# Optimization experiments

Measured on AMD Instinct MI355X. Metric: run time of the kernel, lower is better.

## Reference

```python
import jax, jax.numpy as jnp
import numpy as np

N_ORDER = 256      # HiPPO order (window_size=[256])
OUT_LEN = 96       # output_window_size
IN_LEN = 720       # input_window_size
MULTISCALE = [1, 2, 4]
MODES = 32         # min(32, min(OUT_LEN, IN_LEN)//2)
EPS = 1e-5


def _transition(N):
    Q = np.arange(N, dtype=np.float64)
    R = (2 * Q + 1)[:, None]
    j, i = np.meshgrid(Q, Q)
    A = np.where(i < j, -1.0, (-1.0) ** (i - j + 1)) * R
    B = (-1.0) ** Q[:, None] * R
    return A, B


def _bilinear_discretize(A, B, dt):
    # scipy cont2discrete(method='bilinear'): Ad = (I - dt/2 A)^-1 (I + dt/2 A), Bd = (I - dt/2 A)^-1 dt B
    n = A.shape[0]
    I = np.eye(n)
    ima = I - 0.5 * dt * A
    Ad = np.linalg.solve(ima, I + 0.5 * dt * A)
    Bd = np.linalg.solve(ima, dt * B)
    return Ad, Bd.squeeze(-1)


def _eval_legendre(N, x):
    # Legendre P_n(x), n=0..N-1, via three-term recurrence. Returns [len(x), N].
    P = np.zeros((N, x.shape[0]))
    P[0] = 1.0
    if N > 1:
        P[1] = x
    for n in range(1, N - 1):
        P[n + 1] = ((2 * n + 1) * x * P[n] - n * P[n - 1]) / (n + 1)
    return P.T


def setup_inputs() -> dict:
    key = jax.random.key(0)
    ks = jax.random.split(key, 4)
    B, L, E = 16, IN_LEN, 64
    x = jax.random.normal(ks[0], (B, L, E), dtype=jnp.float32)
    scale = 1.0 / (N_ORDER * N_ORDER)
    wr = scale * jax.random.uniform(ks[1], (3, N_ORDER, N_ORDER, MODES), dtype=jnp.float32)
    wi = scale * jax.random.uniform(ks[2], (3, N_ORDER, N_ORDER, MODES), dtype=jnp.float32)
    mlp_w = 0.1 * jax.random.normal(ks[3], (1, 3), dtype=jnp.float32)
    mlp_b = jnp.zeros((1,), dtype=jnp.float32)
    A_c, B_c = _transition(N_ORDER)
    Ads, Bds, evs = [], [], []
    for m in MULTISCALE:
        dt = 1.0 / OUT_LEN / m
        Ad, Bd = _bilinear_discretize(A_c, B_c, dt)
        vals = np.arange(0.0, 1.0, dt)
        ev = _eval_legendre(N_ORDER, 1.0 - 2.0 * vals)  # [m*OUT_LEN, N]
        Ads.append(Ad); Bds.append(Bd); evs.append(ev[-OUT_LEN:])
    A = jnp.asarray(np.stack(Ads), dtype=jnp.float32)          # [3,N,N]
    Bv = jnp.asarray(np.stack(Bds), dtype=jnp.float32)         # [3,N]
    eval_last = jnp.asarray(np.stack(evs), dtype=jnp.float32)  # [3,OUT_LEN,N]
    return {"x": x, "wr": wr, "wi": wi, "mlp_w": mlp_w, "mlp_b": mlp_b,
            "A": A, "Bv": Bv, "eval_last": eval_last}


def _hippo(xin, Ad, Bd):
    # xin: [B,E,T] -> states [B,E,N,T]; c_t = A c_{t-1} + B f_t
    c0 = jnp.zeros(xin.shape[:2] + (Ad.shape[0],), xin.dtype)
    def step(c, f):  # f: [B,E]
        c = c @ Ad.T + f[..., None] * Bd
        return c, c
    _, cs = jax.lax.scan(step, c0, jnp.moveaxis(xin, -1, 0))  # [T,B,E,N]
    return jnp.transpose(cs, (1, 2, 3, 0))


def _spec_conv(xc, wr, wi):
    # xc: [B,E,N,T]; FFT -> low-mode complex channel mix -> iFFT
    T = xc.shape[-1]
    x_ft = jnp.fft.rfft(xc)                 # [B,E,N,T//2+1]
    a = x_ft[..., :MODES]
    w = (wr + 1j * wi).astype(a.dtype)      # [N,N,MODES]
    out = jnp.einsum('bjix,iox->bjox', a, w)
    nf = T // 2 + 1
    out_ft = jnp.pad(out, ((0, 0), (0, 0), (0, 0), (0, nf - MODES)))
    return jnp.fft.irfft(out_ft, n=T)       # [B,E,N,T]


def reference(x, wr, wi, mlp_w, mlp_b, A, Bv, eval_last):
    # instance standard scale (RevIN-style, no affine)
    mean = jnp.mean(x, axis=1, keepdims=True)            # [B,1,E]
    std = jnp.sqrt(jnp.var(x, axis=1, keepdims=True) + EPS)
    xn = (x - mean) / std
    xe = jnp.transpose(xn, (0, 2, 1))                    # [B,E,L]
    decs = []
    for s, m in enumerate(MULTISCALE):
        T = m * OUT_LEN
        x_in = xe[:, :, -T:]
        xc = _hippo(x_in, A[s], Bv[s])                   # [B,E,N,T]
        out1 = _spec_conv(xc, wr[s], wi[s])              # [B,E,N,T]
        x_dec_c = out1[:, :, :, OUT_LEN - 1]             # [B,E,N]  (input >= output branch, jump_dist=0)
        decs.append(x_dec_c @ eval_last[s].T)            # [B,E,OUT_LEN]
    xd = jnp.stack(decs, axis=-1)                        # [B,E,OUT,3]
    xd = (xd @ mlp_w.T + mlp_b)[..., 0]                  # [B,E,OUT]
    xd = jnp.transpose(xd, (0, 2, 1))                    # [B,OUT,E]
    return xd * std + mean
```

## Files before the change

kernel.cpp:

```cpp
#include <hip/hip_runtime.h>

typedef unsigned short u16;
typedef unsigned int u32;

typedef __bf16 bf16x8 __attribute__((ext_vector_type(8)));
typedef unsigned short ushort8 __attribute__((ext_vector_type(8)));
typedef float f32x16 __attribute__((ext_vector_type(16)));

#define STATSP 2048
#define EPOFF 32768
#define KKOFF0 591872
#define KKOFF1 616448
#define KKOFF2 665600
#define WOFF 763904
#define R0OFF 5482496
#define R1OFF 6072320
#define R2OFF 7251968
#define HTOTOFF 11675648
#define AD64 0
#define PD64 196608
#define KKD64 589824

__device__ __forceinline__ u32 pack_hl(float a) {
  u32 bits = __builtin_bit_cast(u32, a);
  u32 hi = (bits + 0x7fffu + ((bits >> 16) & 1u)) >> 16;
  float hif = __builtin_bit_cast(float, hi << 16);
  float r = a - hif;
  u32 lo = __builtin_bit_cast(u32, r) >> 16;
  return hi | (lo << 16);
}

__device__ __forceinline__ void unpk8(const u32* p, bf16x8& h, bf16x8& l) {
  ushort8 hu, lu;
#pragma unroll
  for (int j = 0; j < 8; ++j) {
    u32 v = p[j];
    hu[j] = (unsigned short)(v & 0xffffu);
    lu[j] = (unsigned short)(v >> 16);
  }
  h = __builtin_bit_cast(bf16x8, hu);
  l = __builtin_bit_cast(bf16x8, lu);
}

__global__ __launch_bounds__(256) void k_pre(const float* __restrict__ Ab,
                                             const float* __restrict__ Bb,
                                             const float* __restrict__ xin,
                                             const float* __restrict__ ev,
                                             float* __restrict__ ws) {
  __shared__ float rs[4][64], rq[4][64];
  int blk = blockIdx.x, tid = threadIdx.x;
  if (blk < 771) {
    double* dws = (double*)(ws + WOFF);
    int idx = blk * 256 + tid;
    if (idx < 196608) {
      dws[AD64 + idx] = (double)Ab[idx];
    } else {
      int g = idx - 196608;
      const int rowoff[3] = {0, 24576, 73728};
      const int kko[3] = {KKOFF0, KKOFF1, KKOFF2};
      int s = g >> 8, i = g & 255;
      float v = Bb[g];
      dws[KKD64 + rowoff[s] + i] = (double)v;
      ((u32*)ws)[kko[s] + i] = pack_hl(v);
    }
  } else if (blk < 963) {
    int b2 = blk - 771;
    int b = b2 / 12, part = b2 % 12;
    int j = tid & 63, g = tid >> 6;
    const float* xp = xin + ((size_t)b * 720 + part * 60 + g) * 64 + j;
    float sum = 0.f, ss = 0.f;
#pragma unroll
    for (int i = 0; i < 15; ++i) {
      float v = xp[(size_t)i * 256];
      sum += v; ss += v * v;
    }
    rs[g][j] = sum; rq[g][j] = ss;
    __syncthreads();
    if (g == 0) {
      float s = rs[0][j] + rs[1][j] + rs[2][j] + rs[3][j];
      float q = rq[0][j] + rq[1][j] + rq[2][j] + rq[3][j];
      float* dst = ws + STATSP + ((size_t)b2 * 64 + j) * 2;
      dst[0] = s; dst[1] = q;
    }
  } else if (blk < 987) {
    int idx = (blk - 963) * 256 + tid;
    for (; idx < 36864; idx += 24 * 256) ws[HTOTOFF + idx] = 0.f;
  } else {
    int idx = (blk - 987) * 256 + tid;
    ((u32*)ws)[EPOFF + idx] = pack_hl(ev[idx]);
  }
}

struct G64Jobs {
  const double* A[8]; const double* B[8]; double* C[8]; float* CF[8];
  int M[8]; int transB[8]; int tile0[8];
  int njobs;
};

__global__ __launch_bounds__(256) void k_gemm64(G64Jobs jb) {
  int bid = blockIdx.x;
  int j = 0;
  for (int q = 1; q < jb.njobs; ++q) if (bid >= jb.tile0[q]) j = q;
  int local = bid - jb.tile0[j];
  int tm = local >> 3, tn = local & 7;
  const double* A = jb.A[j];
  const double* Bm = jb.B[j];
  double* C = jb.C[j];
  float* CF = jb.CF[j];
  int M = jb.M[j], tB = jb.transB[j];
  int row0 = tm * 32, col0 = tn * 32;
  __shared__ double As[32][33], Bs[32][33];
  int tid = threadIdx.x;
  int ty = tid >> 4, tx = tid & 15;
  int lr = tid >> 3, lk = (tid & 7) << 2;
  double va[4], vb[4];
#pragma unroll
  for (int u = 0; u < 4; ++u) {
    va[u] = (row0 + lr < M) ? A[(size_t)(row0 + lr) * 256 + lk + u] : 0.0;
    vb[u] = tB ? Bm[(size_t)(col0 + lr) * 256 + lk + u]
               : Bm[(size_t)lr * 256 + col0 + lk + u];
  }
  double a00 = 0., a01 = 0., a10 = 0., a11 = 0.;
  for (int kc = 0; kc < 256; kc += 32) {
#pragma unroll
    for (int u = 0; u < 4; ++u) {
      As[lr][lk + u] = va[u];
      if (tB) Bs[lk + u][lr] = vb[u];
      else    Bs[lr][lk + u] = vb[u];
    }
    __syncthreads();
    if (kc < 224) {
      int kn = kc + 32;
#pragma unroll
      for (int u = 0; u < 4; ++u) {
        va[u] = (row0 + lr < M) ? A[(size_t)(row0 + lr) * 256 + kn + lk + u] : 0.0;
        vb[u] = tB ? Bm[(size_t)(col0 + lr) * 256 + kn + lk + u]
                   : Bm[(size_t)(kn + lr) * 256 + col0 + lk + u];
      }
    }
#pragma unroll 8
    for (int k = 0; k < 32; ++k) {
      double x0 = As[2 * ty][k], x1 = As[2 * ty + 1][k];
      double y0 = Bs[k][2 * tx], y1 = Bs[k][2 * tx + 1];
      a00 = fma(x0, y0, a00); a01 = fma(x0, y1, a01);
      a10 = fma(x1, y0, a10); a11 = fma(x1, y1, a11);
    }
    __syncthreads();
  }
  int r0 = row0 + 2 * ty, c0 = col0 + 2 * tx;
  if (r0 < M) {
    C[(size_t)r0 * 256 + c0] = a00; C[(size_t)r0 * 256 + c0 + 1] = a01;
    if (CF) {
      ((u32*)CF)[(size_t)r0 * 256 + c0] = pack_hl((float)a00);
      ((u32*)CF)[(size_t)r0 * 256 + c0 + 1] = pack_hl((float)a01);
    }
  }
  if (r0 + 1 < M) {
    C[(size_t)(r0 + 1) * 256 + c0] = a10; C[(size_t)(r0 + 1) * 256 + c0 + 1] = a11;
    if (CF) {
      ((u32*)CF)[(size_t)(r0 + 1) * 256 + c0] = pack_hl((float)a10);
      ((u32*)CF)[(size_t)(r0 + 1) * 256 + c0 + 1] = pack_hl((float)a11);
    }
  }
}

__global__ __launch_bounds__(256, 3) void k_s3(const float* __restrict__ wr,
                                               const float* __restrict__ wi,
                                               float* __restrict__ ws) {
  __shared__ float ms[64 * 97];
  int bid = blockIdx.x;
  int jidx = bid >> 7;
  int r127 = bid & 127;
  int mb = ((r127 & 7) << 4) | (r127 >> 3);
  int s = jidx >> 1, p = jidx & 1;
  const float* w = (p ? wi : wr) + (size_t)s * 2097152;
  const u32* ep = (const u32*)ws + EPOFF + s * 24576;
  int i0 = mb * 2;
  int tid = threadIdx.x;
  int lane = tid & 63;
  int wid = tid >> 6;
  int il = wid & 1, kh = wid >> 1;

  int tcol = lane & 31;
  int og8 = (lane >> 5) << 3;
  const float* aw0 = w + (((size_t)(i0 + il) * 256 + kh * 128 + og8) << 5) + tcol;
  const u32* bsrc = ep + tcol * 256 + og8;

  f32x16 acc[3];
#pragma unroll
  for (int f = 0; f < 3; ++f)
#pragma unroll
    for (int r = 0; r < 16; ++r) acc[f][r] = 0.f;

#pragma unroll 2
  for (int c = 0; c < 4; ++c) {
    int ko = kh * 128 + c * 32;
#pragma unroll
    for (int ks = 0; ks < 2; ++ks) {
      const float* aw = aw0 + ((c * 32 + ks * 16) << 5);
      u32 ap[8];
#pragma unroll
      for (int j2 = 0; j2 < 8; ++j2) ap[j2] = pack_hl(aw[(size_t)j2 << 5]);
      bf16x8 ah, al;
      unpk8(ap, ah, al);
#pragma unroll
      for (int f = 0; f < 3; ++f) {
        const uint4* bq = (const uint4*)(bsrc + f * 8192 + ko + ks * 16);
        uint4 b0 = bq[0], b1 = bq[1];
        u32 bp[8] = {b0.x, b0.y, b0.z, b0.w, b1.x, b1.y, b1.z, b1.w};
        bf16x8 bh, bl;
        unpk8(bp, bh, bl);
        acc[f] = __builtin_amdgcn_mfma_f32_32x32x16_bf16(ah, bh, acc[f], 0, 0, 0);
        acc[f] = __builtin_amdgcn_mfma_f32_32x32x16_bf16(ah, bl, acc[f], 0, 0, 0);
        acc[f] = __builtin_amdgcn_mfma_f32_32x32x16_bf16(al, bh, acc[f], 0, 0, 0);
      }
    }
  }

  int crow0 = (lane >> 5) << 2;
  if (kh == 1) {
#pragma unroll
    for (int f = 0; f < 3; ++f)
#pragma unroll
      for (int r = 0; r < 16; ++r) {
        int row = il * 32 + crow0 + (r & 3) + ((r >> 2) << 3);
        ms[row * 97 + f * 32 + tcol] = acc[f][r];
      }
  }
  __syncthreads();
  if (kh == 0) {
#pragma unroll
    for (int f = 0; f < 3; ++f)
#pragma unroll
      for (int r = 0; r < 16; ++r) {
        int row = il * 32 + crow0 + (r & 3) + ((r >> 2) << 3);
        int a = row * 97 + f * 32 + tcol;
        ms[a] += acc[f][r];
      }
  }
  __syncthreads();
  u32* W2 = (u32*)(ws + WOFF) + (size_t)jidx * 786432 + (size_t)(mb >> 2) * 24576 +
            ((mb & 3) << 1);
  int x = tid & 31, cg = tid >> 5;
#pragma unroll
  for (int j = 0; j < 12; ++j) {
    int c = cg * 12 + j;
    float v0 = ms[x * 97 + c];
    float v1 = ms[(32 + x) * 97 + c];
    uint2 st;
    st.x = pack_hl(v0);
    st.y = pack_hl(v1);
    *(uint2*)(W2 + (size_t)(x * 96 + c) * 8) = st;
  }
}

__global__ __launch_bounds__(256) void k_s4(float* __restrict__ ws) {
  int bid = blockIdx.x;
  const int cums[6] = {0, 36, 72, 144, 216, 360};
  int jidx = 0;
#pragma unroll
  for (int q = 1; q < 6; ++q) if (bid >= cums[q]) jidx = q;
  int local = bid - cums[jidx];
  int s = jidx >> 1, p = jidx & 1;
  const int Ts[3] = {96, 192, 384};
  const int KKo[3] = {KKOFF0, KKOFF1, KKOFF2};
  const int Ro[3] = {R0OFF, R1OFF, R2OFF};
  int T = Ts[s];
  int td = local / 12, tn = local % 12;
  int d0 = td * 32;
  int tid = threadIdx.x;
  int lane = tid & 63, wid = tid >> 6;
  int n0 = tn * 256 + wid * 64;
  int l31 = lane & 31, kg = lane >> 5;
  const u32* Ap = (const u32*)ws + KKo[s] + (size_t)(d0 + l31) * 256 + kg * 8;
  const u32* Bp = (const u32*)ws + WOFF + (size_t)jidx * 786432 + (size_t)kg * 24576;
  const u32* b0p = Bp + (size_t)(n0 + l31) * 8;
  const u32* b1p = Bp + (size_t)(n0 + 32 + l31) * 8;
  float* C = ws + Ro[s] + (size_t)p * T * 3072;

  f32x16 acc0, acc1;
#pragma unroll
  for (int r = 0; r < 16; ++r) { acc0[r] = 0.f; acc1[r] = 0.f; }

#pragma unroll 2
  for (int ks = 0; ks < 16; ++ks) {
    uint4 a0 = *(const uint4*)(Ap + ks * 16);
    uint4 a1 = *(const uint4*)(Ap + ks * 16 + 4);
    size_t bo = (size_t)ks * 49152;
    uint4 x0 = *(const uint4*)(b0p + bo);
    uint4 x1 = *(const uint4*)(b0p + bo + 4);
    uint4 y0 = *(const uint4*)(b1p + bo);
    uint4 y1 = *(const uint4*)(b1p + bo + 4);
    u32 ap[8] = {a0.x, a0.y, a0.z, a0.w, a1.x, a1.y, a1.z, a1.w};
    bf16x8 ah, al;
    unpk8(ap, ah, al);
    {
      u32 bp[8] = {x0.x, x0.y, x0.z, x0.w, x1.x, x1.y, x1.z, x1.w};
      bf16x8 bh, bl;
      unpk8(bp, bh, bl);
      acc0 = __builtin_amdgcn_mfma_f32_32x32x16_bf16(ah, bh, acc0, 0, 0, 0);
      acc0 = __builtin_amdgcn_mfma_f32_32x32x16_bf16(ah, bl, acc0, 0, 0, 0);
      acc0 = __builtin_amdgcn_mfma_f32_32x32x16_bf16(al, bh, acc0, 0, 0, 0);
      acc0 = __builtin_amdgcn_mfma_f32_32x32x16_bf16(al, bl, acc0, 0, 0, 0);
    }
    {
      u32 bp[8] = {y0.x, y0.y, y0.z, y0.w, y1.x, y1.y, y1.z, y1.w};
      bf16x8 bh, bl;
      unpk8(bp, bh, bl);
      acc1 = __builtin_amdgcn_mfma_f32_32x32x16_bf16(ah, bh, acc1, 0, 0, 0);
      acc1 = __builtin_amdgcn_mfma_f32_32x32x16_bf16(ah, bl, acc1, 0, 0, 0);
      acc1 = __builtin_amdgcn_mfma_f32_32x32x16_bf16(al, bh, acc1, 0, 0, 0);
      acc1 = __builtin_amdgcn_mfma_f32_32x32x16_bf16(al, bl, acc1, 0, 0, 0);
    }
  }

  int crow = kg << 2;
#pragma unroll
  for (int r = 0; r < 16; ++r) {
    int row = d0 + crow + (r & 3) + ((r >> 2) << 3);
    C[(size_t)row * 3072 + n0 + l31] = acc0[r];
    C[(size_t)row * 3072 + n0 + 32 + l31] = acc1[r];
  }
}

__global__ __launch_bounds__(192) void k_s5a(const float* __restrict__ mlpw, float* __restrict__ ws) {
  int bid = blockIdx.x;
  int s = bid >> 7;
  int rem = bid & 127;
  int x = rem >> 2;
  int tq = rem & 3;
  const int Ts[3] = {96, 192, 384};
  const int Ro[3] = {R0OFF, R1OFF, R2OFF};
  const int lpbase[3] = {288, 192, 0};
  int T = Ts[s];
  int Lc = T >> 3;
  __shared__ float cs[384][2];
  __shared__ float Lsr[8][24], Lsi[8][24];
  int tid = threadIdx.x;
  for (int e = tid; e < T; e += 192) {
    float th = 6.283185307179586f * (float)e / (float)T;
    cs[e][0] = cosf(th);
    cs[e][1] = sinf(th);
  }
  int c = tid / 24, tl = tid % 24;
  int t = tq * 24 + tl;
  const float* Rre = ws + Ro[s] + (size_t)x * 96 + t;
  const float* Rim = Rre + (size_t)T * 3072;
  float* Htot = ws + HTOTOFF;
  float wsc = mlpw[s];
  __syncthreads();
  int d0 = c * Lc;
  float zr = 0.f, zi = 0.f;
  for (int d = d0; d < d0 + Lc; ++d) {
    float rr = Rre[(size_t)d * 3072];
    float ri = Rim[(size_t)d * 3072];
    int e1 = (x * d) % T;
    float c1 = cs[e1][0], s1 = cs[e1][1];
    zr += c1 * rr + s1 * ri;
    zi += c1 * ri - s1 * rr;
  }
  Lsr[c][tl] = zr; Lsi[c][tl] = zi;
  __syncthreads();
  if (c == 0) {
    float pr = 0.f, pi = 0.f;
#pragma unroll
    for (int cc = 0; cc < 8; ++cc) {
      float lr = Lsr[cc][tl], li = Lsi[cc][tl];
      Lsr[cc][tl] = pr; Lsi[cc][tl] = pi;
      pr += lr; pi += li;
    }
  }
  __syncthreads();
  zr = Lsr[c][tl]; zi = Lsi[c][tl];
  float sc = (((x == 0) ? 1.f : 2.f) / (float)T) * wsc;
  for (int d = d0; d < d0 + Lc; ++d) {
    float rr = Rre[(size_t)d * 3072];
    float ri = Rim[(size_t)d * 3072];
    int e1 = (x * d) % T;
    float c1 = cs[e1][0], s1 = cs[e1][1];
    zr += c1 * rr + s1 * ri;
    zi += c1 * ri - s1 * rr;
    int k = T - 1 - d;
    int e2 = (x * (95 - k)) % T;
    if (e2 < 0) e2 += T;
    float c2 = cs[e2][0], s2 = cs[e2][1];
    atomicAdd(Htot + (size_t)(lpbase[s] + k) * 96 + t, sc * (c2 * zr - s2 * zi));
  }
}

__global__ __launch_bounds__(256) void k_s6(const float* __restrict__ xin, const float* __restrict__ mlpb_p,
                                            const float* __restrict__ ws, float* __restrict__ out) {
  int b = blockIdx.x >> 2, tq = blockIdx.x & 3;
  int tid = threadIdx.x;
  int j = tid & 63, tsub = tid >> 6;
  __shared__ float Ht[384 * 24];
  for (int idx = tid; idx < 384 * 24; idx += 256) {
    int lp = idx / 24, c = idx % 24;
    Ht[idx] = ws[HTOTOFF + lp * 96 + tq * 24 + c];
  }
  float ssum = 0.f, sq = 0.f;
#pragma unroll
  for (int p = 0; p < 12; ++p) {
    const float* src = ws + STATSP + (((size_t)b * 12 + p) * 64 + j) * 2;
    ssum += src[0]; sq += src[1];
  }
  float mn = ssum * (1.f / 720.f);
  float var = sq * (1.f / 720.f) - mn * mn;
  float sd = sqrtf(var + 1e-5f);
  __syncthreads();
  float mlpb = mlpb_p[0];
  float acc[6] = {0.f, 0.f, 0.f, 0.f, 0.f, 0.f};
  float accS[6] = {0.f, 0.f, 0.f, 0.f, 0.f, 0.f};
  const float* xp = xin + ((size_t)b * 720 + 336) * 64 + j;
  for (int lp = 0; lp < 384; ++lp) {
    float xv = xp[(size_t)lp * 64];
    const float* hr = &Ht[lp * 24 + tsub * 6];
    float2 h01 = *(const float2*)&hr[0];
    float2 h23 = *(const float2*)&hr[2];
    float2 h45 = *(const float2*)&hr[4];
    float hh[6] = {h01.x, h01.y, h23.x, h23.y, h45.x, h45.y};
#pragma unroll
    for (int u = 0; u < 6; ++u) {
      acc[u] += xv * hh[u];
      accS[u] += hh[u];
    }
  }
#pragma unroll
  for (int u = 0; u < 6; ++u) {
    int t = tq * 24 + tsub * 6 + u;
    float val = acc[u] + mn * (1.f - accS[u]) + sd * mlpb;
    out[((size_t)b * 96 + t) * 64 + j] = val;
  }
}

extern "C" void kernel_launch(void* const* d_in, const int* in_sizes, int n_in,
                              void* d_out, int out_size, void* d_ws, size_t ws_size,
                              hipStream_t stream) {
  const float* x  = (const float*)d_in[0];
  const float* wr = (const float*)d_in[1];
  const float* wi = (const float*)d_in[2];
  const float* mw = (const float*)d_in[3];
  const float* mb = (const float*)d_in[4];
  const float* Ab = (const float*)d_in[5];
  const float* Bb = (const float*)d_in[6];
  const float* ev = (const float*)d_in[7];
  float* wsf = (float*)d_ws;
  float* out = (float*)d_out;

  k_pre<<<1275, 256, 0, stream>>>(Ab, Bb, x, ev, wsf);

  const double* AD = (const double*)(wsf + WOFF) + AD64;
  double* PD = (double*)(wsf + WOFF) + PD64;
  double* KD = (double*)(wsf + WOFF) + KKD64;
  static const int Ts[3] = {96, 192, 384};
  static const int rowoff[3] = {0, 24576, 73728};
  static const int KKo[3] = {KKOFF0, KKOFF1, KKOFF2};

  int have[3] = {1, 1, 1};
  for (int r = 0; r <= 8; ++r) {
    G64Jobs jb;
    jb.njobs = 0;
    int tiles = 0;
    for (int s = 0; s < 3; ++s) {
      int T = Ts[s];
      if (have[s] >= T) continue;
      const double* Pn = (r == 0) ? (AD + (size_t)s * 65536)
                                  : (PD + (size_t)(2 * s + (r & 1)) * 65536);
      int M = ((2 * have[s] < T) ? 2 * have[s] : T) - have[s];
      int q = jb.njobs++;
      jb.A[q] = KD + rowoff[s]; jb.B[q] = Pn;
      jb.C[q] = KD + rowoff[s] + (size_t)have[s] * 256;
      jb.CF[q] = wsf + KKo[s] + (size_t)have[s] * 256;
      jb.M[q] = M; jb.transB[q] = 1; jb.tile0[q] = tiles;
      tiles += ((M + 31) / 32) * 8;
      if (2 * have[s] < T) {
        q = jb.njobs++;
        jb.A[q] = Pn; jb.B[q] = Pn;
        jb.C[q] = PD + (size_t)(2 * s + ((r + 1) & 1)) * 65536;
        jb.CF[q] = nullptr;
        jb.M[q] = 256; jb.transB[q] = 0; jb.tile0[q] = tiles;
        tiles += 64;
      }
      have[s] = (2 * have[s] < T) ? 2 * have[s] : T;
    }
    if (jb.njobs) k_gemm64<<<tiles, 256, 0, stream>>>(jb);
  }

  k_s3<<<768, 256, 0, stream>>>(wr, wi, wsf);
  k_s4<<<504, 256, 0, stream>>>(wsf);
  k_s5a<<<384, 192, 0, stream>>>(mw, wsf);
  k_s6<<<64, 256, 0, stream>>>(x, mb, wsf, out);
}
```

Before: 376.7 us.

## Split k_s3 work across six waves by output column group and prefetch operands

k_s3 now launches 384 threads (6 waves), each computing one of the three output column groups for one row half over the full K range, instead of 4 waves that split K in half and reduced the halves through shared memory. The K loop is fully unrolled with register double-buffering of the next A and B fragments. The epilogue writes packed results straight from registers, using a smaller shared buffer only to pair the two row halves. This removes the K-split reduction and one barrier, and raises per-block parallelism. In exchange each wave runs a longer serial MFMA chain and needs more registers for prefetching.

```diff
diff --git a/kernel.cpp b/kernel.cpp
--- a/kernel.cpp
+++ b/kernel.cpp
@@ -164,10 +164,10 @@
   }
 }
 
-__global__ __launch_bounds__(256, 3) void k_s3(const float* __restrict__ wr,
-                                               const float* __restrict__ wi,
-                                               float* __restrict__ ws) {
-  __shared__ float ms[64 * 97];
+__global__ __launch_bounds__(384) void k_s3(const float* __restrict__ wr,
+                                            const float* __restrict__ wi,
+                                            float* __restrict__ ws) {
+  __shared__ u32 ls[3168];
   int bid = blockIdx.x;
   int jidx = bid >> 7;
   int r127 = bid & 127;
@@ -179,78 +179,74 @@
   int tid = threadIdx.x;
   int lane = tid & 63;
   int wid = tid >> 6;
-  int il = wid & 1, kh = wid >> 1;
+  int il = wid & 1, f = wid >> 1;
 
   int tcol = lane & 31;
   int og8 = (lane >> 5) << 3;
-  const float* aw0 = w + (((size_t)(i0 + il) * 256 + kh * 128 + og8) << 5) + tcol;
-  const u32* bsrc = ep + tcol * 256 + og8;
-
-  f32x16 acc[3];
-#pragma unroll
-  for (int f = 0; f < 3; ++f)
-#pragma unroll
-    for (int r = 0; r < 16; ++r) acc[f][r] = 0.f;
-
-#pragma unroll 2
-  for (int c = 0; c < 4; ++c) {
-    int ko = kh * 128 + c * 32;
-#pragma unroll
-    for (int ks = 0; ks < 2; ++ks) {
-      const float* aw = aw0 + ((c * 32 + ks * 16) << 5);
-      u32 ap[8];
-#pragma unroll
-      for (int j2 = 0; j2 < 8; ++j2) ap[j2] = pack_hl(aw[(size_t)j2 << 5]);
-      bf16x8 ah, al;
-      unpk8(ap, ah, al);
-#pragma unroll
-      for (int f = 0; f < 3; ++f) {
-        const uint4* bq = (const uint4*)(bsrc + f * 8192 + ko + ks * 16);
-        uint4 b0 = bq[0], b1 = bq[1];
-        u32 bp[8] = {b0.x, b0.y, b0.z, b0.w, b1.x, b1.y, b1.z, b1.w};
-        bf16x8 bh, bl;
-        unpk8(bp, bh, bl);
-        acc[f] = __builtin_amdgcn_mfma_f32_32x32x16_bf16(ah, bh, acc[f], 0, 0, 0);
-        acc[f] = __builtin_amdgcn_mfma_f32_32x32x16_bf16(ah, bl, acc[f], 0, 0, 0);
-        acc[f] = __builtin_amdgcn_mfma_f32_32x32x16_bf16(al, bh, acc[f], 0, 0, 0);
-      }
-    }
-  }
-
-  int crow0 = (lane >> 5) << 2;
-  if (kh == 1) {
-#pragma unroll
-    for (int f = 0; f < 3; ++f)
-#pragma unroll
-      for (int r = 0; r < 16; ++r) {
-        int row = il * 32 + crow0 + (r & 3) + ((r >> 2) << 3);
-        ms[row * 97 + f * 32 + tcol] = acc[f][r];
-      }
+  const float* aw0 = w + (((size_t)(i0 + il) * 256 + og8) << 5) + tcol;
+  const u32* bsrc = ep + (size_t)(f * 32 + tcol) * 256 + og8;
+
+  f32x16 acc;
+#pragma unroll
+  for (int r = 0; r < 16; ++r) acc[r] = 0.f;
+
+  float fa[8]; uint4 vb0, vb1;
+#pragma unroll
+  for (int j = 0; j < 8; ++j) fa[j] = aw0[(size_t)j << 5];
+  vb0 = *(const uint4*)(bsrc);
+  vb1 = *(const uint4*)(bsrc + 4);
+
+#pragma unroll
+  for (int ks = 0; ks < 16; ++ks) {
+    float fan[8]; uint4 nb0, nb1;
+    if (ks < 15) {
+      const float* awn = aw0 + ((size_t)(ks + 1) << 9);
+#pragma unroll
+      for (int j = 0; j < 8; ++j) fan[j] = awn[(size_t)j << 5];
+      nb0 = *(const uint4*)(bsrc + (ks + 1) * 16);
+      nb1 = *(const uint4*)(bsrc + (ks + 1) * 16 + 4);
+    }
+    u32 ap[8];
+#pragma unroll
+    for (int j = 0; j < 8; ++j) ap[j] = pack_hl(fa[j]);
+    bf16x8 ah, al;
+    unpk8(ap, ah, al);
+    u32 bp[8] = {vb0.x, vb0.y, vb0.z, vb0.w, vb1.x, vb1.y, vb1.z, vb1.w};
+    bf16x8 bh, bl;
+    unpk8(bp, bh, bl);
+    acc = __builtin_amdgcn_mfma_f32_32x32x16_bf16(ah, bh, acc, 0, 0, 0);
+    acc = __builtin_amdgcn_mfma_f32_32x32x16_bf16(ah, bl, acc, 0, 0, 0);
+    acc = __builtin_amdgcn_mfma_f32_32x32x16_bf16(al, bh, acc, 0, 0, 0);
+    if (ks < 15) {
+#pragma unroll
+      for (int j = 0; j < 8; ++j) fa[j] = fan[j];
+      vb0 = nb0; vb1 = nb1;
+    }
+  }
+
+  int x0 = (lane >> 5) << 2;
+  u32 mine[16];
+#pragma unroll
+  for (int r = 0; r < 16; ++r) mine[r] = pack_hl(acc[r]);
+  if (il == 0) {
+#pragma unroll
+    for (int r = 0; r < 16; ++r) {
+      int row = x0 + (r & 3) + ((r >> 2) << 3);
+      ls[f * 1056 + row * 33 + tcol] = mine[r];
+    }
   }
   __syncthreads();
-  if (kh == 0) {
-#pragma unroll
-    for (int f = 0; f < 3; ++f)
-#pragma unroll
-      for (int r = 0; r < 16; ++r) {
-        int row = il * 32 + crow0 + (r & 3) + ((r >> 2) << 3);
-        int a = row * 97 + f * 32 + tcol;
-        ms[a] += acc[f][r];
-      }
-  }
-  __syncthreads();
-  u32* W2 = (u32*)(ws + WOFF) + (size_t)jidx * 786432 + (size_t)(mb >> 2) * 24576 +
-            ((mb & 3) << 1);
-  int x = tid & 31, cg = tid >> 5;
-#pragma unroll
-  for (int j = 0; j < 12; ++j) {
-    int c = cg * 12 + j;
-    float v0 = ms[x * 97 + c];
-    float v1 = ms[(32 + x) * 97 + c];
-    uint2 st;
-    st.x = pack_hl(v0);
-    st.y = pack_hl(v1);
-    *(uint2*)(W2 + (size_t)(x * 96 + c) * 8) = st;
+  if (il == 1) {
+    u32* W2 = (u32*)(ws + WOFF) + (size_t)jidx * 786432 +
+              (size_t)(mb >> 2) * 24576 + ((mb & 3) << 1);
+#pragma unroll
+    for (int r = 0; r < 16; ++r) {
+      int row = x0 + (r & 3) + ((r >> 2) << 3);
+      uint2 st;
+      st.x = ls[f * 1056 + row * 33 + tcol];
+      st.y = mine[r];
+      *(uint2*)(W2 + (size_t)(row * 96 + f * 32 + tcol) * 8) = st;
+    }
   }
 }
 
@@ -486,7 +482,7 @@
     if (jb.njobs) k_gemm64<<<tiles, 256, 0, stream>>>(jb);
   }
 
-  k_s3<<<768, 256, 0, stream>>>(wr, wi, wsf);
+  k_s3<<<768, 384, 0, stream>>>(wr, wi, wsf);
   k_s4<<<504, 256, 0, stream>>>(wsf);
   k_s5a<<<384, 192, 0, stream>>>(mw, wsf);
   k_s6<<<64, 256, 0, stream>>>(x, mb, wsf, out);
```

New measurement: 384.2 us. About the same (+2.0%).
